# Kernel tuning notes

Measured on AMD Instinct MI355X. Metric: run time of the kernel, lower is better.

The kernel has to match this reference:

```python
import jax, jax.numpy as jnp
import numpy as np

GROUP_SIZE = 128


def setup_inputs() -> dict:
    key = jax.random.key(0)
    k0, k1, k2, k3 = jax.random.split(key, 4)
    B, S, I, O, G = 4, 2048, 4096, 11008, GROUP_SIZE
    x = jax.random.normal(k0, (B, S, I), dtype=jnp.float32)
    # int4 values in [-8, 7]
    qweight = jax.random.randint(k1, (O, I), -8, 8, dtype=jnp.int32)
    # group-wise positive scales, shape [O, I // G]
    scales = jax.random.uniform(k2, (O, I // G), dtype=jnp.float32,
                                minval=1e-3, maxval=2e-2)
    bias = jax.random.normal(k3, (O,), dtype=jnp.float32) * 0.01
    return {"x": x, "qweight": qweight, "scales": scales, "bias": bias}


def reference(x, qweight, scales, bias):
    # bits == 4, quantized path: group-wise dequant then linear
    O, I = qweight.shape
    G = GROUP_SIZE
    w = qweight.reshape(O, I // G, G).astype(x.dtype) * scales[:, :, None].astype(x.dtype)
    w = w.reshape(O, I)  # dequantized weight [O, I]
    # F.linear: y = x @ w.T + bias
    return jnp.einsum('bsi,oi->bso', x, w) + bias.astype(x.dtype)
```

## Files before the change

kernel.cpp:

```cpp
#include <hip/hip_runtime.h>
#include <hip/hip_bf16.h>


typedef __bf16 bf16_t;
typedef __bf16 bf16x8 __attribute__((ext_vector_type(8)));
typedef float f32x4 __attribute__((ext_vector_type(4)));
typedef int ix4 __attribute__((ext_vector_type(4)));
typedef __attribute__((address_space(3))) unsigned char lds_byte;
typedef __attribute__((address_space(1))) unsigned char gmem_byte;

__global__ void rowmax_kernel(const float* __restrict__ x, float* __restrict__ sx, int I) {
  __shared__ float red[256];
  const int m = blockIdx.x;
  const float* row = x + (size_t)m * I;
  float mx = 0.f;
  for (int c = threadIdx.x * 4; c < I; c += 256 * 4) {
    const float4 f = *reinterpret_cast<const float4*>(row + c);
    mx = fmaxf(mx, fmaxf(fmaxf(fabsf(f.x), fabsf(f.y)), fmaxf(fabsf(f.z), fabsf(f.w))));
  }
  red[threadIdx.x] = mx;
  __syncthreads();
#pragma unroll
  for (int s = 128; s > 0; s >>= 1) {
    if (threadIdx.x < s) red[threadIdx.x] = fmaxf(red[threadIdx.x], red[threadIdx.x + s]);
    __syncthreads();
  }
  if (threadIdx.x == 0) sx[m] = fmaxf(red[0], 1e-30f) * (1.f / 127.f);
}

__global__ void quant_x_kernel(const float* __restrict__ x, const float* __restrict__ sx,
                               int* __restrict__ xq, int I16, long n16) {
  const long stride = (long)gridDim.x * blockDim.x;
  for (long i = (long)blockIdx.x * blockDim.x + threadIdx.x; i < n16; i += stride) {
    const int m = (int)(i / I16);
    const float inv = 1.f / sx[m];
    const float4* p = reinterpret_cast<const float4*>(x + i * 16);
    int b[16];
#pragma unroll
    for (int c = 0; c < 4; ++c) {
      const float4 f = p[c];
      b[c * 4 + 0] = (int)rintf(f.x * inv);
      b[c * 4 + 1] = (int)rintf(f.y * inv);
      b[c * 4 + 2] = (int)rintf(f.z * inv);
      b[c * 4 + 3] = (int)rintf(f.w * inv);
    }
    int4 o;
    o.x = (b[0] & 255) | ((b[1] & 255) << 8) | ((b[2] & 255) << 16) | (b[3] << 24);
    o.y = (b[4] & 255) | ((b[5] & 255) << 8) | ((b[6] & 255) << 16) | (b[7] << 24);
    o.z = (b[8] & 255) | ((b[9] & 255) << 8) | ((b[10] & 255) << 16) | (b[11] << 24);
    o.w = (b[12] & 255) | ((b[13] & 255) << 8) | ((b[14] & 255) << 16) | (b[15] << 24);
    reinterpret_cast<int4*>(xq)[i] = o;
  }
}

__global__ void colscale_kernel(const float* __restrict__ sc, float* __restrict__ tw,
                                int NG, int O) {
  const int n = blockIdx.x * blockDim.x + threadIdx.x;
  if (n >= O) return;
  const float* row = sc + (size_t)n * NG;
  float mx = 0.f;
  for (int g = 0; g < NG; ++g) mx = fmaxf(mx, row[g]);
  tw[n] = fmaxf(mx, 1e-30f) * (8.f / 127.f);
}

__global__ void quant_w_kernel(const int* __restrict__ qw, const float* __restrict__ sc,
                               const float* __restrict__ tw, int* __restrict__ wq,
                               int I, int G, long n16) {
  const long stride = (long)gridDim.x * blockDim.x;
  const int I16 = I / 16;
  for (long i = (long)blockIdx.x * blockDim.x + threadIdx.x; i < n16; i += stride) {
    const int n = (int)(i / I16);
    const int k0 = (int)((i - (long)n * I16) * 16);
    const float f = sc[(size_t)n * (I / G) + k0 / G] / tw[n];
    const int4* p = reinterpret_cast<const int4*>(qw + (size_t)n * I + k0);
    const int4 q0 = p[0], q1 = p[1], q2 = p[2], q3 = p[3];
    int b[16];
    b[0] = (int)rintf((float)q0.x * f); b[1] = (int)rintf((float)q0.y * f);
    b[2] = (int)rintf((float)q0.z * f); b[3] = (int)rintf((float)q0.w * f);
    b[4] = (int)rintf((float)q1.x * f); b[5] = (int)rintf((float)q1.y * f);
    b[6] = (int)rintf((float)q1.z * f); b[7] = (int)rintf((float)q1.w * f);
    b[8] = (int)rintf((float)q2.x * f); b[9] = (int)rintf((float)q2.y * f);
    b[10] = (int)rintf((float)q2.z * f); b[11] = (int)rintf((float)q2.w * f);
    b[12] = (int)rintf((float)q3.x * f); b[13] = (int)rintf((float)q3.y * f);
    b[14] = (int)rintf((float)q3.z * f); b[15] = (int)rintf((float)q3.w * f);
    int4 o;
    o.x = (b[0] & 255) | ((b[1] & 255) << 8) | ((b[2] & 255) << 16) | (b[3] << 24);
    o.y = (b[4] & 255) | ((b[5] & 255) << 8) | ((b[6] & 255) << 16) | (b[7] << 24);
    o.z = (b[8] & 255) | ((b[9] & 255) << 8) | ((b[10] & 255) << 16) | (b[11] << 24);
    o.w = (b[12] & 255) | ((b[13] & 255) << 8) | ((b[14] & 255) << 16) | (b[15] << 24);
    reinterpret_cast<int4*>(wq)[i] = o;
  }
}


#define WAITV(n) asm volatile("s_waitcnt vmcnt(" #n ")" ::: "memory")
#define WAITL(n) asm volatile("s_waitcnt lgkmcnt(" #n ")" ::: "memory")
#define BAR() __builtin_amdgcn_s_barrier()
#define SETP(n) __builtin_amdgcn_s_setprio(n)

#define RD_A(DB, q) do { \
  _Pragma("unroll") \
  for (int i_ = 0; i_ < 4; ++i_) { \
    aF[i_][0] = *reinterpret_cast<const ix4*>(&ldsb[(DB) + aRd + (unsigned)((q) * 64 + i_ * 16) * 128u + ks0]); \
    aF[i_][1] = *reinterpret_cast<const ix4*>(&ldsb[(DB) + aRd + (unsigned)((q) * 64 + i_ * 16) * 128u + ks1]); \
  } \
} while (0)

#define RD_B(DB, nh, BF) do { \
  _Pragma("unroll") \
  for (int j_ = 0; j_ < 2; ++j_) { \
    BF[j_][0] = *reinterpret_cast<const ix4*>(&ldsb[(DB) + bRd + (unsigned)((nh) * 32 + j_ * 16) * 128u + ks0]); \
    BF[j_][1] = *reinterpret_cast<const ix4*>(&ldsb[(DB) + bRd + (unsigned)((nh) * 32 + j_ * 16) * 128u + ks1]); \
  } \
} while (0)

#define STG(BASE, P, tau) do { \
  __builtin_amdgcn_global_load_lds((const gmem_byte*)((P) + (size_t)(tau) * 128), \
                                   (lds_byte*)&ldsb[(BASE) + wOff], 16, 0, 0); \
  __builtin_amdgcn_global_load_lds((const gmem_byte*)((P) + (size_t)64 * K + (size_t)(tau) * 128), \
                                   (lds_byte*)&ldsb[(BASE) + 8192u + wOff], 16, 0, 0); \
} while (0)

#define MMQI(q, nh, BF) do { \
  _Pragma("unroll") \
  for (int i_ = 0; i_ < 4; ++i_) \
  _Pragma("unroll") \
  for (int j_ = 0; j_ < 2; ++j_) { \
    acc[(q) * 4 + i_][(nh) * 2 + j_] = __builtin_amdgcn_mfma_i32_16x16x64_i8(aF[i_][0], BF[j_][0], acc[(q) * 4 + i_][(nh) * 2 + j_], 0, 0, 0); \
    acc[(q) * 4 + i_][(nh) * 2 + j_] = __builtin_amdgcn_mfma_i32_16x16x64_i8(aF[i_][1], BF[j_][1], acc[(q) * 4 + i_][(nh) * 2 + j_], 0, 0, 0); \
  } \
} while (0)

__launch_bounds__(512, 2)
__global__ void gemm256_i8_kernel(const char* __restrict__ A, const char* __restrict__ B,
                                  const float* __restrict__ sx, const float* __restrict__ tw,
                                  const float* __restrict__ bias, float* __restrict__ C,
                                  int M, int N, int K) {
  __shared__ __align__(16) unsigned char ldsb[131072];

  const int tid = threadIdx.x;
  const int lane = tid & 63;
  const int w = tid >> 6;
  const int wr = w >> 2;
  const int wc = w & 3;

  const int MT = M >> 8;
  int mt, nt;
  const int bid = blockIdx.x;
  if ((MT & 7) == 0) {
    const int xcd = bid & 7, idx = bid >> 3;
    const int mpx = MT >> 3;
    nt = idx / mpx;
    mt = xcd * mpx + (idx - nt * mpx);
  } else {
    mt = bid % MT;
    nt = bid / MT;
  }
  const int m0 = mt << 8, n0 = nt << 8;

  const int srow8 = lane >> 3;
  const int scol16 = (lane & 7) ^ (srow8 & 7);
  const char* aP0 = A + (size_t)(m0 + w * 8 + srow8) * K + scol16 * 16;
  const char* aP1 = aP0 + (size_t)128 * K;
  const char* bP0 = B + (size_t)(n0 + w * 8 + srow8) * K + scol16 * 16;
  const char* bP1 = bP0 + (size_t)128 * K;
  const unsigned wOff = (unsigned)w * 1024u;

  const unsigned fr = lane & 15;
  const unsigned hi16 = (unsigned)lane >> 4;
  const unsigned sw_ = (fr & 7u) << 4;
  const unsigned ks0 = (hi16 * 16u) ^ sw_;
  const unsigned ks1 = (64u + hi16 * 16u) ^ sw_;
  const unsigned aRd = (unsigned)wr * 16384u + fr * 128u;
  const unsigned bRd = 32768u + (unsigned)(wc >> 1) * 16384u +
                       ((unsigned)(wc & 1) * 64u + fr) * 128u;

  ix4 acc[8][4];
#pragma unroll
  for (int i = 0; i < 8; ++i)
#pragma unroll
    for (int j = 0; j < 4; ++j) acc[i][j] = (ix4){0, 0, 0, 0};

  ix4 aF[4][2], bF0[2][2], bF1[2][2];

  const int NITER = K >> 8;

  STG(0u, aP0, 0); STG(32768u, bP0, 0); STG(49152u, bP1, 0); STG(16384u, aP1, 0);
  STG(98304u, bP0, 1); STG(114688u, bP1, 1); STG(65536u, aP0, 1);
  WAITV(6);
  BAR();

  for (int it = 0; it < NITER - 1; ++it) {
    const int t = 2 * it;
    RD_A(0u, 0); RD_B(0u, 0, bF0); RD_B(0u, 1, bF1); STG(81920u, aP1, t + 1);
    BAR(); WAITL(0);
    SETP(1); MMQI(0, 0, bF0); SETP(0); BAR();
    STG(32768u, bP0, t + 2);
    BAR();
    SETP(1); MMQI(0, 1, bF1); SETP(0); BAR();
    RD_A(0u, 1); STG(49152u, bP1, t + 2);
    BAR(); WAITL(0);
    SETP(1); MMQI(1, 0, bF0); SETP(0); BAR();
    STG(0u, aP0, t + 2); WAITV(6);
    BAR();
    SETP(1); MMQI(1, 1, bF1); SETP(0); BAR();
    RD_A(65536u, 0); RD_B(65536u, 0, bF0); RD_B(65536u, 1, bF1); STG(16384u, aP1, t + 2);
    BAR(); WAITL(0);
    SETP(1); MMQI(0, 0, bF0); SETP(0); BAR();
    STG(98304u, bP0, t + 3);
    BAR();
    SETP(1); MMQI(0, 1, bF1); SETP(0); BAR();
    RD_A(65536u, 1); STG(114688u, bP1, t + 3);
    BAR(); WAITL(0);
    SETP(1); MMQI(1, 0, bF0); SETP(0); BAR();
    STG(65536u, aP0, t + 3); WAITV(6);
    BAR();
    SETP(1); MMQI(1, 1, bF1); SETP(0); BAR();
  }
  {
    const int t = 2 * NITER - 2;
    RD_A(0u, 0); RD_B(0u, 0, bF0); RD_B(0u, 1, bF1); STG(81920u, aP1, t + 1);
    BAR(); WAITL(0);
    SETP(1); MMQI(0, 0, bF0); SETP(0); BAR();
    BAR();
    SETP(1); MMQI(0, 1, bF1); SETP(0); BAR();
    RD_A(0u, 1);
    BAR(); WAITL(0);
    SETP(1); MMQI(1, 0, bF0); SETP(0); BAR();
    WAITV(0);
    BAR();
    SETP(1); MMQI(1, 1, bF1); SETP(0); BAR();
    RD_A(65536u, 0); RD_B(65536u, 0, bF0); RD_B(65536u, 1, bF1);
    WAITL(0);
    SETP(1); MMQI(0, 0, bF0); SETP(0);
    SETP(1); MMQI(0, 1, bF1); SETP(0);
    RD_A(65536u, 1);
    WAITL(0);
    SETP(1); MMQI(1, 0, bF0); SETP(0);
    SETP(1); MMQI(1, 1, bF1); SETP(0);
  }

  const int row0 = m0 + wr * 128 + ((lane >> 4) << 2);
  const int col0 = n0 + wc * 64 + (lane & 15);
  float sxc[8][4];
#pragma unroll
  for (int hi = 0; hi < 8; ++hi) {
    const int rbase = row0 + (hi >> 2) * 64 + (hi & 3) * 16;
#pragma unroll
    for (int r = 0; r < 4; ++r) sxc[hi][r] = sx[rbase + r];
  }
#pragma unroll
  for (int j = 0; j < 4; ++j) {
    const int n = col0 + j * 16;
    const float tn = tw[n];
    const float bv = bias[n];
#pragma unroll
    for (int hi = 0; hi < 8; ++hi) {
      const int rbase = row0 + (hi >> 2) * 64 + (hi & 3) * 16;
#pragma unroll
      for (int r = 0; r < 4; ++r)
        C[(size_t)(rbase + r) * N + n] = sxc[hi][r] * tn * (float)acc[hi][j][r] + bv;
    }
  }
}

__global__ void cvt_x_kernel(const float* __restrict__ x, bf16_t* __restrict__ xb, long n8) {
  const long stride = (long)gridDim.x * blockDim.x;
  for (long i = (long)blockIdx.x * blockDim.x + threadIdx.x; i < n8; i += stride) {
    const float4* p = reinterpret_cast<const float4*>(x + i * 8);
    const float4 f0 = p[0];
    const float4 f1 = p[1];
    bf16x8 o;
    o[0] = (bf16_t)f0.x; o[1] = (bf16_t)f0.y; o[2] = (bf16_t)f0.z; o[3] = (bf16_t)f0.w;
    o[4] = (bf16_t)f1.x; o[5] = (bf16_t)f1.y; o[6] = (bf16_t)f1.z; o[7] = (bf16_t)f1.w;
    *reinterpret_cast<bf16x8*>(xb + i * 8) = o;
  }
}

__global__ void deq_w_kernel(const int* __restrict__ qw, const float* __restrict__ sc,
                             bf16_t* __restrict__ wb, int I, int G) {
  const int n = blockIdx.y;
  const int kb = blockIdx.x * blockDim.x + threadIdx.x;
  const int k = kb * 8;
  if (k >= I) return;
  const float s = sc[(size_t)n * (I / G) + k / G];
  const int4* qp = reinterpret_cast<const int4*>(qw + (size_t)n * I + k);
  const int4 q0 = qp[0];
  const int4 q1 = qp[1];
  bf16x8 o;
  o[0] = (bf16_t)((float)q0.x * s);
  o[1] = (bf16_t)((float)q0.y * s);
  o[2] = (bf16_t)((float)q0.z * s);
  o[3] = (bf16_t)((float)q0.w * s);
  o[4] = (bf16_t)((float)q1.x * s);
  o[5] = (bf16_t)((float)q1.y * s);
  o[6] = (bf16_t)((float)q1.z * s);
  o[7] = (bf16_t)((float)q1.w * s);
  *reinterpret_cast<bf16x8*>(wb + (size_t)n * I + k) = o;
}

#define BM 128
#define BK 32
__launch_bounds__(256)
__global__ void gemm_bt_kernel(const bf16_t* __restrict__ A, const bf16_t* __restrict__ B,
                               const float* __restrict__ bias, float* __restrict__ C,
                               int M, int N, int K) {
  __shared__ __align__(16) bf16_t As[2][BM * BK];
  __shared__ __align__(16) bf16_t Bs[2][BM * BK];
  const int tid = threadIdx.x;
  const int lane = tid & 63;
  const int w = tid >> 6;
  const int wr = w >> 1;
  const int wc = w & 1;
  const int m0 = blockIdx.y * BM;
  const int n0 = blockIdx.x * BM;
  const int srow = lane >> 2;
  const int schunk = lane & 3;
  f32x4 acc[4][4];
  const f32x4 zero = {0.f, 0.f, 0.f, 0.f};
#pragma unroll
  for (int i = 0; i < 4; ++i)
#pragma unroll
    for (int j = 0; j < 4; ++j) acc[i][j] = zero;
  const int nt = K / BK;
  auto stage = [&](int t, int buf) {
    const int k0 = t * BK;
#pragma unroll
    for (int j = 0; j < 2; ++j) {
      const int row = w * 32 + j * 16;
      const bf16_t* ga = A + (size_t)(m0 + row + srow) * K + k0 + schunk * 8;
      __builtin_amdgcn_global_load_lds((const gmem_byte*)ga, (lds_byte*)&As[buf][row * BK], 16, 0, 0);
      const bf16_t* gb = B + (size_t)(n0 + row + srow) * K + k0 + schunk * 8;
      __builtin_amdgcn_global_load_lds((const gmem_byte*)gb, (lds_byte*)&Bs[buf][row * BK], 16, 0, 0);
    }
  };
  auto compute = [&](int buf) {
    bf16x8 af[4], bfr[4];
    const int fr2 = lane & 15;
    const int kc = (lane >> 4) * 8;
#pragma unroll
    for (int i = 0; i < 4; ++i) {
      af[i] = *reinterpret_cast<const bf16x8*>(&As[buf][(wr * 64 + i * 16 + fr2) * BK + kc]);
      bfr[i] = *reinterpret_cast<const bf16x8*>(&Bs[buf][(wc * 64 + i * 16 + fr2) * BK + kc]);
    }
#pragma unroll
    for (int i = 0; i < 4; ++i)
#pragma unroll
      for (int j = 0; j < 4; ++j)
        acc[i][j] = __builtin_amdgcn_mfma_f32_16x16x32_bf16(af[i], bfr[j], acc[i][j], 0, 0, 0);
  };
  stage(0, 0);
  __syncthreads();
  int cur = 0;
  for (int t = 0; t < nt - 1; ++t) {
    stage(t + 1, cur ^ 1);
    compute(cur);
    __syncthreads();
    cur ^= 1;
  }
  compute(cur);
#pragma unroll
  for (int j = 0; j < 4; ++j) {
    const int n = n0 + wc * 64 + j * 16 + (lane & 15);
    const float bv = bias[n];
#pragma unroll
    for (int i = 0; i < 4; ++i) {
      const int mbase = m0 + wr * 64 + i * 16 + (lane >> 4) * 4;
#pragma unroll
      for (int r = 0; r < 4; ++r)
        C[(size_t)(mbase + r) * N + n] = acc[i][j][r] + bv;
    }
  }
}

extern "C" void kernel_launch(void* const* d_in, const int* in_sizes, int n_in,
                              void* d_out, int out_size, void* d_ws, size_t ws_size,
                              hipStream_t stream) {
  const float* x = (const float*)d_in[0];
  const int* qw = (const int*)d_in[1];
  const float* sc = (const float*)d_in[2];
  const float* bias = (const float*)d_in[3];
  float* out = (float*)d_out;

  const long O = in_sizes[3];
  const long I = in_sizes[1] / O;
  const long M = in_sizes[0] / I;
  const long G = I / (in_sizes[2] / O);
  const long NG = I / G;

  const size_t i8need = (size_t)(M + O) * I + 4 * (size_t)(M + O);
  const bool i8ok = ((M & 255) == 0) && ((O & 255) == 0) && ((I & 255) == 0) &&
                    (G == 128) && ((I >> 8) >= 2) && ((I & 3) == 0) &&
                    (ws_size >= i8need);
  if (i8ok) {
    char* xq = (char*)d_ws;
    char* wq = xq + (size_t)M * I;
    float* sx = (float*)(wq + (size_t)O * I);
    float* tw = sx + M;
    rowmax_kernel<<<(unsigned)M, 256, 0, stream>>>(x, sx, (int)I);
    quant_x_kernel<<<2048, 256, 0, stream>>>(x, sx, (int*)xq, (int)(I / 16), M * I / 16);
    colscale_kernel<<<(unsigned)((O + 255) / 256), 256, 0, stream>>>(sc, tw, (int)NG, (int)O);
    quant_w_kernel<<<2048, 256, 0, stream>>>(qw, sc, tw, (int*)wq, (int)I, (int)G, O * I / 16);
    const int nwg = (int)((M >> 8) * (O >> 8));
    gemm256_i8_kernel<<<nwg, 512, 0, stream>>>(xq, wq, sx, tw, bias, out, (int)M, (int)O, (int)I);
  } else {
    bf16_t* xb = (bf16_t*)d_ws;
    bf16_t* wb = xb + (size_t)M * I;
    if (ws_size < (size_t)(M + O) * I * sizeof(bf16_t)) return;
    cvt_x_kernel<<<2048, 256, 0, stream>>>(x, xb, M * I / 8);
    dim3 dgrid((unsigned)((I / 8 + 255) / 256), (unsigned)O);
    deq_w_kernel<<<dgrid, 256, 0, stream>>>(qw, sc, wb, (int)I, (int)G);
    dim3 ggrid((unsigned)(O / BM), (unsigned)(M / BM));
    gemm_bt_kernel<<<ggrid, 256, 0, stream>>>(xb, wb, bias, out, (int)M, (int)O, (int)I);
  }
}
```

Before: 512.1 us.

## Fuse x row-max and int8 quantization, restructure GEMM main-loop staging schedule

Merges the row-max and x quantization kernels into one per-row kernel that re-reads the row (likely from cache) and writes packed int8, removing a launch and a separate pass over x. The int8 GEMM main loop is rescheduled: global-to-LDS stages are issued in pairs, two MFMA groups are batched between barriers, and the number of barriers and vmcnt waits per iteration is roughly halved. Fewer barriers let more MFMAs issue back to back, but prefetch distance changes and the wait counts must still match the outstanding loads, so the ordering needs care.

```diff
diff --git a/kernel.cpp b/kernel.cpp
--- a/kernel.cpp
+++ b/kernel.cpp
@@ -9,12 +9,13 @@
 typedef __attribute__((address_space(3))) unsigned char lds_byte;
 typedef __attribute__((address_space(1))) unsigned char gmem_byte;
 
-__global__ void rowmax_kernel(const float* __restrict__ x, float* __restrict__ sx, int I) {
+__global__ void rowquant_kernel(const float* __restrict__ x, int* __restrict__ xq,
+                                float* __restrict__ sx, int I) {
   __shared__ float red[256];
   const int m = blockIdx.x;
   const float* row = x + (size_t)m * I;
   float mx = 0.f;
-  for (int c = threadIdx.x * 4; c < I; c += 256 * 4) {
+  for (int c = threadIdx.x * 4; c < I; c += 1024) {
     const float4 f = *reinterpret_cast<const float4*>(row + c);
     mx = fmaxf(mx, fmaxf(fmaxf(fabsf(f.x), fabsf(f.y)), fmaxf(fabsf(f.z), fabsf(f.w))));
   }
@@ -25,31 +26,15 @@
     if (threadIdx.x < s) red[threadIdx.x] = fmaxf(red[threadIdx.x], red[threadIdx.x + s]);
     __syncthreads();
   }
-  if (threadIdx.x == 0) sx[m] = fmaxf(red[0], 1e-30f) * (1.f / 127.f);
-}
-
-__global__ void quant_x_kernel(const float* __restrict__ x, const float* __restrict__ sx,
-                               int* __restrict__ xq, int I16, long n16) {
-  const long stride = (long)gridDim.x * blockDim.x;
-  for (long i = (long)blockIdx.x * blockDim.x + threadIdx.x; i < n16; i += stride) {
-    const int m = (int)(i / I16);
-    const float inv = 1.f / sx[m];
-    const float4* p = reinterpret_cast<const float4*>(x + i * 16);
-    int b[16];
-#pragma unroll
-    for (int c = 0; c < 4; ++c) {
-      const float4 f = p[c];
-      b[c * 4 + 0] = (int)rintf(f.x * inv);
-      b[c * 4 + 1] = (int)rintf(f.y * inv);
-      b[c * 4 + 2] = (int)rintf(f.z * inv);
-      b[c * 4 + 3] = (int)rintf(f.w * inv);
-    }
-    int4 o;
-    o.x = (b[0] & 255) | ((b[1] & 255) << 8) | ((b[2] & 255) << 16) | (b[3] << 24);
-    o.y = (b[4] & 255) | ((b[5] & 255) << 8) | ((b[6] & 255) << 16) | (b[7] << 24);
-    o.z = (b[8] & 255) | ((b[9] & 255) << 8) | ((b[10] & 255) << 16) | (b[11] << 24);
-    o.w = (b[12] & 255) | ((b[13] & 255) << 8) | ((b[14] & 255) << 16) | (b[15] << 24);
-    reinterpret_cast<int4*>(xq)[i] = o;
+  const float rm = fmaxf(red[0], 1e-30f);
+  if (threadIdx.x == 0) sx[m] = rm * (1.f / 127.f);
+  const float inv = 127.f / rm;
+  int* orow = xq + (size_t)m * (I >> 2);
+  for (int c = threadIdx.x * 4; c < I; c += 1024) {
+    const float4 f = *reinterpret_cast<const float4*>(row + c);
+    const int b0 = (int)rintf(f.x * inv), b1 = (int)rintf(f.y * inv);
+    const int b2 = (int)rintf(f.z * inv), b3 = (int)rintf(f.w * inv);
+    orow[c >> 2] = (b0 & 255) | ((b1 & 255) << 8) | ((b2 & 255) << 16) | (b3 << 24);
   }
 }
 
@@ -185,59 +170,47 @@
 
   const int NITER = K >> 8;
 
-  STG(0u, aP0, 0); STG(32768u, bP0, 0); STG(49152u, bP1, 0); STG(16384u, aP1, 0);
-  STG(98304u, bP0, 1); STG(114688u, bP1, 1); STG(65536u, aP0, 1);
-  WAITV(6);
+  STG(0u, aP0, 0); STG(16384u, aP1, 0); STG(32768u, bP0, 0); STG(49152u, bP1, 0);
+  STG(98304u, bP0, 1); STG(114688u, bP1, 1);
+  WAITV(4);
   BAR();
 
   for (int it = 0; it < NITER - 1; ++it) {
     const int t = 2 * it;
-    RD_A(0u, 0); RD_B(0u, 0, bF0); RD_B(0u, 1, bF1); STG(81920u, aP1, t + 1);
-    BAR(); WAITL(0);
-    SETP(1); MMQI(0, 0, bF0); SETP(0); BAR();
-    STG(32768u, bP0, t + 2);
-    BAR();
-    SETP(1); MMQI(0, 1, bF1); SETP(0); BAR();
-    RD_A(0u, 1); STG(49152u, bP1, t + 2);
-    BAR(); WAITL(0);
-    SETP(1); MMQI(1, 0, bF0); SETP(0); BAR();
-    STG(0u, aP0, t + 2); WAITV(6);
-    BAR();
-    SETP(1); MMQI(1, 1, bF1); SETP(0); BAR();
-    RD_A(65536u, 0); RD_B(65536u, 0, bF0); RD_B(65536u, 1, bF1); STG(16384u, aP1, t + 2);
-    BAR(); WAITL(0);
-    SETP(1); MMQI(0, 0, bF0); SETP(0); BAR();
-    STG(98304u, bP0, t + 3);
-    BAR();
-    SETP(1); MMQI(0, 1, bF1); SETP(0); BAR();
-    RD_A(65536u, 1); STG(114688u, bP1, t + 3);
-    BAR(); WAITL(0);
-    SETP(1); MMQI(1, 0, bF0); SETP(0); BAR();
-    STG(65536u, aP0, t + 3); WAITV(6);
-    BAR();
-    SETP(1); MMQI(1, 1, bF1); SETP(0); BAR();
+    RD_A(0u, 0); RD_B(0u, 0, bF0); RD_B(0u, 1, bF1);
+    STG(65536u, aP0, t + 1); STG(81920u, aP1, t + 1);
+    BAR(); WAITL(0);
+    SETP(1); MMQI(0, 0, bF0); MMQI(0, 1, bF1); SETP(0); BAR();
+    RD_A(0u, 1);
+    STG(32768u, bP0, t + 2); STG(49152u, bP1, t + 2);
+    WAITV(4);
+    BAR(); WAITL(0);
+    SETP(1); MMQI(1, 0, bF0); MMQI(1, 1, bF1); SETP(0); BAR();
+    RD_A(65536u, 0); RD_B(65536u, 0, bF0); RD_B(65536u, 1, bF1);
+    STG(0u, aP0, t + 2); STG(16384u, aP1, t + 2);
+    BAR(); WAITL(0);
+    SETP(1); MMQI(0, 0, bF0); MMQI(0, 1, bF1); SETP(0); BAR();
+    RD_A(65536u, 1);
+    STG(98304u, bP0, t + 3); STG(114688u, bP1, t + 3);
+    WAITV(4);
+    BAR(); WAITL(0);
+    SETP(1); MMQI(1, 0, bF0); MMQI(1, 1, bF1); SETP(0); BAR();
   }
   {
-    const int t = 2 * NITER - 2;
-    RD_A(0u, 0); RD_B(0u, 0, bF0); RD_B(0u, 1, bF1); STG(81920u, aP1, t + 1);
-    BAR(); WAITL(0);
-    SETP(1); MMQI(0, 0, bF0); SETP(0); BAR();
-    BAR();
-    SETP(1); MMQI(0, 1, bF1); SETP(0); BAR();
+    RD_A(0u, 0); RD_B(0u, 0, bF0); RD_B(0u, 1, bF1);
+    STG(65536u, aP0, 2 * NITER - 1); STG(81920u, aP1, 2 * NITER - 1);
+    BAR(); WAITL(0);
+    SETP(1); MMQI(0, 0, bF0); MMQI(0, 1, bF1); SETP(0); BAR();
     RD_A(0u, 1);
-    BAR(); WAITL(0);
-    SETP(1); MMQI(1, 0, bF0); SETP(0); BAR();
     WAITV(0);
-    BAR();
-    SETP(1); MMQI(1, 1, bF1); SETP(0); BAR();
+    BAR(); WAITL(0);
+    SETP(1); MMQI(1, 0, bF0); MMQI(1, 1, bF1); SETP(0); BAR();
     RD_A(65536u, 0); RD_B(65536u, 0, bF0); RD_B(65536u, 1, bF1);
     WAITL(0);
-    SETP(1); MMQI(0, 0, bF0); SETP(0);
-    SETP(1); MMQI(0, 1, bF1); SETP(0);
+    SETP(1); MMQI(0, 0, bF0); MMQI(0, 1, bF1); SETP(0);
     RD_A(65536u, 1);
     WAITL(0);
-    SETP(1); MMQI(1, 0, bF0); SETP(0);
-    SETP(1); MMQI(1, 1, bF1); SETP(0);
+    SETP(1); MMQI(1, 0, bF0); MMQI(1, 1, bF1); SETP(0);
   }
 
   const int row0 = m0 + wr * 128 + ((lane >> 4) << 2);
@@ -390,15 +363,14 @@
 
   const size_t i8need = (size_t)(M + O) * I + 4 * (size_t)(M + O);
   const bool i8ok = ((M & 255) == 0) && ((O & 255) == 0) && ((I & 255) == 0) &&
-                    (G == 128) && ((I >> 8) >= 2) && ((I & 3) == 0) &&
+                    (G == 128) && ((I >> 8) >= 2) &&
                     (ws_size >= i8need);
   if (i8ok) {
     char* xq = (char*)d_ws;
     char* wq = xq + (size_t)M * I;
     float* sx = (float*)(wq + (size_t)O * I);
     float* tw = sx + M;
-    rowmax_kernel<<<(unsigned)M, 256, 0, stream>>>(x, sx, (int)I);
-    quant_x_kernel<<<2048, 256, 0, stream>>>(x, sx, (int*)xq, (int)(I / 16), M * I / 16);
+    rowquant_kernel<<<(unsigned)M, 256, 0, stream>>>(x, (int*)xq, sx, (int)I);
     colscale_kernel<<<(unsigned)((O + 255) / 256), 256, 0, stream>>>(sc, tw, (int)NG, (int)O);
     quant_w_kernel<<<2048, 256, 0, stream>>>(qw, sc, tw, (int*)wq, (int)I, (int)G, O * I / 16);
     const int nwg = (int)((M >> 8) * (O >> 8));
```

After: 496.5 us. 3.0% less time.
